# Performance work log

Hardware: AMD Instinct MI355X
Metric: run time of the kernel (lower is better)

## Reference

```python
import jax, jax.numpy as jnp
import numpy as np

B, G, P, E, H, K = 16, 512, 512, 256, 16, 16
CLIP = 10.0

def setup_inputs() -> dict:
    key = jax.random.key(0)
    ks = jax.random.split(key, 10)
    d = {
        "input1": jax.random.normal(ks[0], (B, 1, E), jnp.float32),
        "input2": jax.random.normal(ks[1], (B, G, E), jnp.float32),
        "current_time": jax.random.uniform(ks[2], (B, G, 1), jnp.float32),
        "ninf_mask": jnp.zeros((B, G, P), jnp.float32),
        "encoded_nodes": jax.random.normal(ks[3], (B, P, E), jnp.float32),
        # learned params (Linear weights stored [in, out]; y = x @ W)
        "Wq": jax.random.normal(ks[4], (2 * E + 1, H * K), jnp.float32) / np.sqrt(2 * E + 1),
        "Wk": jax.random.normal(ks[5], (E, H * K), jnp.float32) / np.sqrt(E),
        "Wv": jax.random.normal(ks[6], (E, H * K), jnp.float32) / np.sqrt(E),
        "Wc_w": jax.random.normal(ks[7], (H * K, E), jnp.float32) / np.sqrt(H * K),
        "Wc_b": jax.random.normal(ks[8], (E,), jnp.float32) * 0.01,
    }
    return d

def _heads(x):  # [B, N, H*K] -> [B, H, N, K]
    b, n, _ = x.shape
    return x.reshape(b, n, H, K).transpose(0, 2, 1, 3)

def reference(input1, input2, current_time, ninf_mask, encoded_nodes, Wq, Wk, Wv, Wc_w, Wc_b):
    # reset(): precompute k, v, single_head_key from encoded_nodes
    k = _heads(encoded_nodes @ Wk)  # [B,H,P,K]
    v = _heads(encoded_nodes @ Wv)  # [B,H,P,K]

    # forward()
    input_cat = jnp.concatenate(
        (jnp.broadcast_to(input1, (B, G, E)), input2, current_time), axis=2)  # [B,G,2E+1]
    q = _heads(input_cat @ Wq)  # [B,H,G,K]

    # MHA with additive ninf mask
    score = jnp.einsum("bhgk,bhpk->bhgp", q, k) / np.sqrt(K)
    score = score + ninf_mask[:, None, :, :]
    weights = jax.nn.softmax(score, axis=3)
    out = jnp.einsum("bhgp,bhpk->bhgk", weights, v)
    out_concat = out.transpose(0, 2, 1, 3).reshape(B, G, H * K)
    mh_atten_out = out_concat @ Wc_w + Wc_b  # [B,G,E]

    # single-head pointer score with tanh clipping
    score2 = jnp.einsum("bge,bpe->bgp", mh_atten_out, encoded_nodes) / np.sqrt(E)
    score_clipped = CLIP * jnp.tanh(score2)
    probs = jax.nn.softmax(score_clipped + ninf_mask, axis=2)
    return probs
```

## Files before the change

kernel.cpp:

```cpp
#include <hip/hip_runtime.h>
#include <math.h>

#define BB 16
#define GG 512
#define PP 512
#define EE 256
#define HH 16
#define KD 16
#define HK 256

typedef __bf16 bf16x8 __attribute__((ext_vector_type(8)));
typedef __bf16 bf16x4 __attribute__((ext_vector_type(4)));
typedef float f32x4 __attribute__((ext_vector_type(4)));
typedef float f32x16 __attribute__((ext_vector_type(16)));

#define SA_STRIDE 40
#define SMEM_BYTES 30720

__device__ inline void cvt_split8(const float* __restrict__ p, bf16x8& h, bf16x8& l)
{
    float4 f0 = *(const float4*)p;
    float4 f1 = *(const float4*)(p + 4);
    float v[8] = {f0.x, f0.y, f0.z, f0.w, f1.x, f1.y, f1.z, f1.w};
#pragma unroll
    for (int j = 0; j < 8; ++j) {
        __bf16 hh = (__bf16)v[j];
        h[j] = hh;
        l[j] = (__bf16)(v[j] - (float)hh);
    }
}

__global__ __launch_bounds__(256) void weight_prep(const float* __restrict__ Wk,
                                                   const float* __restrict__ Wv,
                                                   const float* __restrict__ Wq,
                                                   const float* __restrict__ Wc,
                                                   const float* __restrict__ in1,
                                                   __bf16* __restrict__ wkt_h, __bf16* __restrict__ wkt_l,
                                                   __bf16* __restrict__ wvt_h, __bf16* __restrict__ wvt_l,
                                                   __bf16* __restrict__ wqt_h, __bf16* __restrict__ wqt_l,
                                                   __bf16* __restrict__ wct_h, __bf16* __restrict__ wct_l,
                                                   float* __restrict__ q1p)
{
    int gid = blockIdx.x * 256 + threadIdx.x;
    if (gid < 16384) {
        const int b = gid >> 10, q = (gid >> 8) & 3, n = gid & 255;
        const float* ip = in1 + (size_t)b * EE + q * 64;
        const float* wp = Wq + (size_t)(q * 64) * HK + n;
        float acc = 0.f;
#pragma unroll 8
        for (int k = 0; k < 64; ++k) acc += ip[k] * wp[(size_t)k * HK];
        q1p[gid] = acc;
        return;
    }
    int id = gid - 16384;
    const float* W;
    __bf16 *th, *tl;
    int krow = 0;
    if (id < 65536)       { W = Wk; th = wkt_h; tl = wkt_l; }
    else if (id < 131072) { id -= 65536;  W = Wv; th = wvt_h; tl = wvt_l; }
    else if (id < 196608) { id -= 131072; W = Wq; th = wqt_h; tl = wqt_l; krow = 256; }
    else                  { id -= 196608; W = Wc; th = wct_h; tl = wct_l; }
    const int k = id & 255;
    const int n = id >> 8;
    const float v = W[(size_t)(k + krow) * HK + n];
    const __bf16 h = (__bf16)v;
    th[(n << 8) + k] = h;
    tl[(n << 8) + k] = (__bf16)(v - (float)h);
}

__device__ inline void kvproj_body(int bx, int tid, unsigned char* smem,
                                   const float* __restrict__ A,
                                   const __bf16* __restrict__ Bkh,
                                   const __bf16* __restrict__ Bkl,
                                   const __bf16* __restrict__ Bvh,
                                   const __bf16* __restrict__ Bvl,
                                   __bf16* __restrict__ Khi,
                                   __bf16* __restrict__ Klo,
                                   __bf16* __restrict__ Vt)
{
    __bf16* sAh = (__bf16*)smem;
    __bf16* sAl = sAh + 64 * SA_STRIDE;
    __bf16* sB  = sAl + 64 * SA_STRIDE;

    const int lane = tid & 63;
    const int w = __builtin_amdgcn_readfirstlane(tid >> 6);
    const int m0 = (bx >> 2) * 64;
    const int n0 = (bx & 3) * 64;
    const int wm = (w >> 1) * 32, wn = (w & 1) * 32;
    const int ln = lane & 15, kq = (lane >> 4) * 8;
    const int ar = tid >> 2, ac = (tid & 3) * 8;

    const __bf16* bsel = (w == 0) ? Bkh : (w == 1) ? Bkl : (w == 2) ? Bvh : Bvl;

    f32x4 ak[2][2], av[2][2];
#pragma unroll
    for (int i = 0; i < 2; ++i)
#pragma unroll
        for (int j = 0; j < 2; ++j) {
            ak[i][j] = (f32x4){0.f, 0.f, 0.f, 0.f};
            av[i][j] = (f32x4){0.f, 0.f, 0.f, 0.f};
        }

    for (int k0 = 0; k0 < EE; k0 += 32) {
        {
            bf16x8 h8, l8;
            cvt_split8(A + (size_t)(m0 + ar) * EE + k0 + ac, h8, l8);
            *(bf16x8*)&sAh[ar * SA_STRIDE + ac] = h8;
            *(bf16x8*)&sAl[ar * SA_STRIDE + ac] = l8;
        }
        {
            const __bf16* src = bsel + (size_t)(n0 + lane) * EE + k0;
            __bf16* dst = sB + (w * 64 + lane) * SA_STRIDE;
            *(bf16x8*)&dst[0]  = *(const bf16x8*)&src[0];
            *(bf16x8*)&dst[8]  = *(const bf16x8*)&src[8];
            *(bf16x8*)&dst[16] = *(const bf16x8*)&src[16];
            *(bf16x8*)&dst[24] = *(const bf16x8*)&src[24];
        }
        __syncthreads();

        bf16x8 ah[2], al[2];
#pragma unroll
        for (int mt = 0; mt < 2; ++mt) {
            ah[mt] = *(const bf16x8*)&sAh[(wm + mt * 16 + ln) * SA_STRIDE + kq];
            al[mt] = *(const bf16x8*)&sAl[(wm + mt * 16 + ln) * SA_STRIDE + kq];
        }
#pragma unroll
        for (int nt = 0; nt < 2; ++nt) {
            const int rowb = wn + nt * 16 + ln;
            bf16x8 bkh8 = *(const bf16x8*)&sB[(0 * 64 + rowb) * SA_STRIDE + kq];
            bf16x8 bkl8 = *(const bf16x8*)&sB[(1 * 64 + rowb) * SA_STRIDE + kq];
            bf16x8 bvh8 = *(const bf16x8*)&sB[(2 * 64 + rowb) * SA_STRIDE + kq];
            bf16x8 bvl8 = *(const bf16x8*)&sB[(3 * 64 + rowb) * SA_STRIDE + kq];
#pragma unroll
            for (int mt = 0; mt < 2; ++mt) {
                ak[mt][nt] = __builtin_amdgcn_mfma_f32_16x16x32_bf16(ah[mt], bkh8, ak[mt][nt], 0, 0, 0);
                ak[mt][nt] = __builtin_amdgcn_mfma_f32_16x16x32_bf16(al[mt], bkh8, ak[mt][nt], 0, 0, 0);
                ak[mt][nt] = __builtin_amdgcn_mfma_f32_16x16x32_bf16(ah[mt], bkl8, ak[mt][nt], 0, 0, 0);
                av[mt][nt] = __builtin_amdgcn_mfma_f32_16x16x32_bf16(ah[mt], bvh8, av[mt][nt], 0, 0, 0);
                av[mt][nt] = __builtin_amdgcn_mfma_f32_16x16x32_bf16(al[mt], bvh8, av[mt][nt], 0, 0, 0);
                av[mt][nt] = __builtin_amdgcn_mfma_f32_16x16x32_bf16(ah[mt], bvl8, av[mt][nt], 0, 0, 0);
            }
        }
        __syncthreads();
    }

    __bf16* eKh = (__bf16*)smem;
    __bf16* eKl = eKh + 5120;
    __bf16* eV  = eKl + 5120;

    const int rbase = (lane >> 4) * 4;
#pragma unroll
    for (int mt = 0; mt < 2; ++mt)
#pragma unroll
        for (int nt = 0; nt < 2; ++nt) {
            const int hloc = (w & 1) * 2 + nt;
            const int nl = wn + nt * 16 + ln;
#pragma unroll
            for (int r = 0; r < 4; ++r) {
                const int m = wm + mt * 16 + rbase + r;
                const float vk = ak[mt][nt][r];
                const __bf16 hk = (__bf16)vk;
                eKh[(hloc * 64 + m) * 20 + ln] = hk;
                eKl[(hloc * 64 + m) * 20 + ln] = (__bf16)(vk - (float)hk);
                eV[nl * 68 + m] = (__bf16)av[mt][nt][r];
            }
        }
    __syncthreads();

    const int b = m0 >> 9;
    const int pbase = m0 & (PP - 1);
    {
        const int hl = tid >> 6, p = tid & 63;
        const int hg = (n0 >> 4) + hl;
        const size_t dst = (((size_t)b * HH + hg) * PP + pbase + p) * KD;
        const int base = (hl * 64 + p) * 20;
        uint2 a0 = *(const uint2*)&eKh[base + 0];
        uint2 a1 = *(const uint2*)&eKh[base + 4];
        uint2 a2 = *(const uint2*)&eKh[base + 8];
        uint2 a3 = *(const uint2*)&eKh[base + 12];
        *(uint4*)(Khi + dst)     = make_uint4(a0.x, a0.y, a1.x, a1.y);
        *(uint4*)(Khi + dst + 8) = make_uint4(a2.x, a2.y, a3.x, a3.y);
        uint2 c0 = *(const uint2*)&eKl[base + 0];
        uint2 c1 = *(const uint2*)&eKl[base + 4];
        uint2 c2 = *(const uint2*)&eKl[base + 8];
        uint2 c3 = *(const uint2*)&eKl[base + 12];
        *(uint4*)(Klo + dst)     = make_uint4(c0.x, c0.y, c1.x, c1.y);
        *(uint4*)(Klo + dst + 8) = make_uint4(c2.x, c2.y, c3.x, c3.y);
    }
    {
        const int n = tid >> 2, qq = tid & 3;
        const int ng = n0 + n, hg = ng >> 4, kk = ng & 15;
        const int base = n * 68 + qq * 16;
        uint2 v0 = *(const uint2*)&eV[base + 0];
        uint2 v1 = *(const uint2*)&eV[base + 4];
        uint2 v2 = *(const uint2*)&eV[base + 8];
        uint2 v3 = *(const uint2*)&eV[base + 12];
        const size_t dst = ((((size_t)b * HH + hg) * KD + kk) * PP) + pbase + qq * 16;
        *(uint4*)(Vt + dst)     = make_uint4(v0.x, v0.y, v1.x, v1.y);
        *(uint4*)(Vt + dst + 8) = make_uint4(v2.x, v2.y, v3.x, v3.y);
    }
}

__device__ inline void qproj_body(int bx, int tid, unsigned char* smem,
                                  const float* __restrict__ in2,
                                  const float* __restrict__ ct,
                                  const __bf16* __restrict__ Bh,
                                  const __bf16* __restrict__ Bl,
                                  const float* __restrict__ WqFull,
                                  const float* __restrict__ q1p,
                                  __bf16* __restrict__ Qhi,
                                  __bf16* __restrict__ Qlo)
{
    __bf16* sAh = (__bf16*)smem;
    __bf16* sAl = sAh + 64 * SA_STRIDE;
    __bf16* sB  = sAl + 64 * SA_STRIDE;

    const int lane = tid & 63;
    const int w = __builtin_amdgcn_readfirstlane(tid >> 6);
    const int m0 = (bx >> 2) * 64;
    const int n0 = (bx & 3) * 64;
    const int wm = (w >> 1) * 32, wn = (w & 1) * 32;
    const int ln = lane & 15, kq = (lane >> 4) * 8;
    const int ar = tid >> 2, ac = (tid & 3) * 8;
    const int b = m0 >> 9;
    const float* WqLast = WqFull + (size_t)512 * HK;

    f32x4 acc[2][2];
#pragma unroll
    for (int i = 0; i < 2; ++i)
#pragma unroll
        for (int j = 0; j < 2; ++j) acc[i][j] = (f32x4){0.f, 0.f, 0.f, 0.f};

    for (int k0 = 0; k0 < EE; k0 += 32) {
        {
            bf16x8 h8, l8;
            cvt_split8(in2 + (size_t)(m0 + ar) * EE + k0 + ac, h8, l8);
            *(bf16x8*)&sAh[ar * SA_STRIDE + ac] = h8;
            *(bf16x8*)&sAl[ar * SA_STRIDE + ac] = l8;
        }
        {
            const int mat = w >> 1;
            const int row = (w & 1) * 32 + (lane >> 1);
            const int half = (lane & 1) * 16;
            const __bf16* src = (mat ? Bl : Bh) + ((size_t)(n0 + row) << 8) + k0 + half;
            __bf16* dst = sB + (mat * 64 + row) * SA_STRIDE + half;
            *(bf16x8*)&dst[0] = *(const bf16x8*)&src[0];
            *(bf16x8*)&dst[8] = *(const bf16x8*)&src[8];
        }
        __syncthreads();

        bf16x8 ah[2], al[2];
#pragma unroll
        for (int mt = 0; mt < 2; ++mt) {
            ah[mt] = *(const bf16x8*)&sAh[(wm + mt * 16 + ln) * SA_STRIDE + kq];
            al[mt] = *(const bf16x8*)&sAl[(wm + mt * 16 + ln) * SA_STRIDE + kq];
        }
#pragma unroll
        for (int nt = 0; nt < 2; ++nt) {
            const int rowb = wn + nt * 16 + ln;
            bf16x8 bh8 = *(const bf16x8*)&sB[(0 * 64 + rowb) * SA_STRIDE + kq];
            bf16x8 bl8 = *(const bf16x8*)&sB[(1 * 64 + rowb) * SA_STRIDE + kq];
#pragma unroll
            for (int mt = 0; mt < 2; ++mt) {
                acc[mt][nt] = __builtin_amdgcn_mfma_f32_16x16x32_bf16(ah[mt], bh8, acc[mt][nt], 0, 0, 0);
                acc[mt][nt] = __builtin_amdgcn_mfma_f32_16x16x32_bf16(al[mt], bh8, acc[mt][nt], 0, 0, 0);
                acc[mt][nt] = __builtin_amdgcn_mfma_f32_16x16x32_bf16(ah[mt], bl8, acc[mt][nt], 0, 0, 0);
            }
        }
        __syncthreads();
    }

    __bf16* eQh = (__bf16*)smem;
    __bf16* eQl = eQh + 5120;

    const int rbase = (lane >> 4) * 4;
#pragma unroll
    for (int mt = 0; mt < 2; ++mt)
#pragma unroll
        for (int nt = 0; nt < 2; ++nt) {
            const int hloc = (w & 1) * 2 + nt;
            const int ng = n0 + wn + nt * 16 + ln;
            const float wq = WqLast[ng];
            const float q1v = q1p[b * 1024 + 0 * 256 + ng] + q1p[b * 1024 + 1 * 256 + ng]
                            + q1p[b * 1024 + 2 * 256 + ng] + q1p[b * 1024 + 3 * 256 + ng];
#pragma unroll
            for (int r = 0; r < 4; ++r) {
                const int m = wm + mt * 16 + rbase + r;
                const float v = acc[mt][nt][r] + q1v + ct[m0 + m] * wq;
                const __bf16 h = (__bf16)v;
                eQh[(hloc * 64 + m) * 20 + ln] = h;
                eQl[(hloc * 64 + m) * 20 + ln] = (__bf16)(v - (float)h);
            }
        }
    __syncthreads();

    {
        const int hl = tid >> 6, p = tid & 63;
        const int hg = (n0 >> 4) + hl;
        const int g = (m0 & (GG - 1)) + p;
        const size_t dst = (((size_t)b * HH + hg) * GG + g) * KD;
        const int base = (hl * 64 + p) * 20;
        uint2 a0 = *(const uint2*)&eQh[base + 0];
        uint2 a1 = *(const uint2*)&eQh[base + 4];
        uint2 a2 = *(const uint2*)&eQh[base + 8];
        uint2 a3 = *(const uint2*)&eQh[base + 12];
        *(uint4*)(Qhi + dst)     = make_uint4(a0.x, a0.y, a1.x, a1.y);
        *(uint4*)(Qhi + dst + 8) = make_uint4(a2.x, a2.y, a3.x, a3.y);
        uint2 c0 = *(const uint2*)&eQl[base + 0];
        uint2 c1 = *(const uint2*)&eQl[base + 4];
        uint2 c2 = *(const uint2*)&eQl[base + 8];
        uint2 c3 = *(const uint2*)&eQl[base + 12];
        *(uint4*)(Qlo + dst)     = make_uint4(c0.x, c0.y, c1.x, c1.y);
        *(uint4*)(Qlo + dst + 8) = make_uint4(c2.x, c2.y, c3.x, c3.y);
    }
}

__global__ __launch_bounds__(256, 2) void fused_proj(const float* __restrict__ enc,
                                                     const __bf16* __restrict__ Bkh,
                                                     const __bf16* __restrict__ Bkl,
                                                     const __bf16* __restrict__ Bvh,
                                                     const __bf16* __restrict__ Bvl,
                                                     __bf16* __restrict__ Khi,
                                                     __bf16* __restrict__ Klo,
                                                     __bf16* __restrict__ Vt,
                                                     const float* __restrict__ in2,
                                                     const float* __restrict__ ct,
                                                     const __bf16* __restrict__ Bqh,
                                                     const __bf16* __restrict__ Bql,
                                                     const float* __restrict__ WqFull,
                                                     const float* __restrict__ q1p,
                                                     __bf16* __restrict__ Qhi,
                                                     __bf16* __restrict__ Qlo)
{
    __shared__ __align__(16) unsigned char smem[SMEM_BYTES];
    const int id = blockIdx.x;
    if (id < 512)
        kvproj_body(id, threadIdx.x, smem, enc, Bkh, Bkl, Bvh, Bvl, Khi, Klo, Vt);
    else
        qproj_body(id - 512, threadIdx.x, smem, in2, ct, Bqh, Bql, WqFull, q1p, Qhi, Qlo);
}

__global__ __launch_bounds__(256, 4) void attn_v8(const __bf16* __restrict__ Qhi,
                                                  const __bf16* __restrict__ Qlo,
                                                  const __bf16* __restrict__ Khi,
                                                  const __bf16* __restrict__ Klo,
                                                  const __bf16* __restrict__ Vt,
                                                  const float* __restrict__ mask,
                                                  __bf16* __restrict__ Ath,
                                                  __bf16* __restrict__ Atl)
{
    __shared__ __align__(16) __bf16 sP[4][32][40];
    __shared__ float srs[4][32];

    const int t = threadIdx.x;
    const int lane = t & 63;
    const int w = __builtin_amdgcn_readfirstlane(t >> 6);
    const int g0 = blockIdx.x * 32;
    const int h = blockIdx.y * 4 + w;
    const int b = blockIdx.z;
    const int ln32 = lane & 31;
    const int half = lane >> 5;
    const int ln16 = lane & 15;
    const int quad = (lane >> 4) & 3;

    const size_t qbase = (((size_t)b * HH + h) * GG + g0) * KD;
    const size_t kbase = ((size_t)b * HH + h) * PP * KD;
    const size_t vbase = ((size_t)b * HH + h) * KD * PP;
    const float* mbase = mask + ((size_t)(b * GG + g0)) * PP;

    bf16x8 qah = *(const bf16x8*)(Qhi + qbase + (size_t)ln32 * KD + half * 8);
    bf16x8 qal = *(const bf16x8*)(Qlo + qbase + (size_t)ln32 * KD + half * 8);

    float rs[16];
#pragma unroll
    for (int r = 0; r < 16; ++r) rs[r] = 0.f;
    f32x4 o0 = (f32x4){0.f, 0.f, 0.f, 0.f};
    f32x4 o1 = (f32x4){0.f, 0.f, 0.f, 0.f};

#pragma unroll 2
    for (int pc = 0; pc < 16; ++pc) {
        const int pb = pc * 32;
        const size_t ko = kbase + (size_t)(pb + ln32) * KD + half * 8;
        bf16x8 kh = *(const bf16x8*)(Khi + ko);
        bf16x8 kl = *(const bf16x8*)(Klo + ko);

        f32x16 s = (f32x16){0.f, 0.f, 0.f, 0.f, 0.f, 0.f, 0.f, 0.f,
                            0.f, 0.f, 0.f, 0.f, 0.f, 0.f, 0.f, 0.f};
        s = __builtin_amdgcn_mfma_f32_32x32x16_bf16(qah, kh, s, 0, 0, 0);
        s = __builtin_amdgcn_mfma_f32_32x32x16_bf16(qal, kh, s, 0, 0, 0);
        s = __builtin_amdgcn_mfma_f32_32x32x16_bf16(qah, kl, s, 0, 0, 0);

#pragma unroll
        for (int r = 0; r < 16; ++r) {
            const int row = (r & 3) + 8 * (r >> 2) + 4 * half;
            const float m = mbase[(size_t)row * PP + pb + ln32];
            const float e = __expf(s[r] * 0.25f + m);
            rs[r] += e;
            sP[w][row][ln32] = (__bf16)e;
        }

        bf16x8 vb = *(const bf16x8*)(Vt + vbase + (size_t)ln16 * PP + pb + quad * 8);
        bf16x8 p0 = *(const bf16x8*)&sP[w][ln16][quad * 8];
        bf16x8 p1 = *(const bf16x8*)&sP[w][16 + ln16][quad * 8];
        o0 = __builtin_amdgcn_mfma_f32_16x16x32_bf16(p0, vb, o0, 0, 0, 0);
        o1 = __builtin_amdgcn_mfma_f32_16x16x32_bf16(p1, vb, o1, 0, 0, 0);
    }

#pragma unroll
    for (int r = 0; r < 16; ++r) {
#pragma unroll
        for (int mm = 1; mm < 32; mm <<= 1) rs[r] += __shfl_xor(rs[r], mm);
    }
    if (ln32 == 0) {
#pragma unroll
        for (int r = 0; r < 16; ++r)
            srs[w][(r & 3) + 8 * (r >> 2) + 4 * half] = rs[r];
    }

#pragma unroll
    for (int t2 = 0; t2 < 2; ++t2) {
        const f32x4 oc = t2 ? o1 : o0;
#pragma unroll
        for (int r = 0; r < 4; ++r) {
            const int grow = t2 * 16 + quad * 4 + r;
            const float v = oc[r] / srs[w][grow];
            const __bf16 hv = (__bf16)v;
            const size_t oo = ((size_t)(b * GG + g0 + grow)) * HK + h * KD + ln16;
            Ath[oo] = hv;
            Atl[oo] = (__bf16)(v - (float)hv);
        }
    }
}

__device__ inline void outproj_body(int bx, int tid,
                                    const __bf16* __restrict__ Ah,
                                    const __bf16* __restrict__ Al,
                                    const __bf16* __restrict__ Bh,
                                    const __bf16* __restrict__ Bl,
                                    const float* __restrict__ bias,
                                    __bf16* __restrict__ Ch,
                                    __bf16* __restrict__ Cl)
{
    const int lane = tid & 63, w = tid >> 6;
    const int m0 = (bx >> 2) * 64 + (w >> 1) * 32;
    const int n0 = (bx & 3) * 64 + (w & 1) * 32;
    const int ln = lane & 15, kc = (lane >> 4) * 8;

    f32x4 acc[2][2];
#pragma unroll
    for (int i = 0; i < 2; ++i)
#pragma unroll
        for (int j = 0; j < 2; ++j) acc[i][j] = (f32x4){0.f, 0.f, 0.f, 0.f};

    for (int k0 = 0; k0 < EE; k0 += 32) {
        bf16x8 ah[2], al[2], bh[2], bl[2];
#pragma unroll
        for (int mt = 0; mt < 2; ++mt) {
            const size_t o = (size_t)(m0 + mt * 16 + ln) * EE + k0 + kc;
            ah[mt] = *(const bf16x8*)(Ah + o);
            al[mt] = *(const bf16x8*)(Al + o);
        }
#pragma unroll
        for (int nt = 0; nt < 2; ++nt) {
            const size_t o = (size_t)(n0 + nt * 16 + ln) * EE + k0 + kc;
            bh[nt] = *(const bf16x8*)(Bh + o);
            bl[nt] = *(const bf16x8*)(Bl + o);
        }
#pragma unroll
        for (int mt = 0; mt < 2; ++mt)
#pragma unroll
            for (int nt = 0; nt < 2; ++nt) {
                acc[mt][nt] = __builtin_amdgcn_mfma_f32_16x16x32_bf16(ah[mt], bh[nt], acc[mt][nt], 0, 0, 0);
                acc[mt][nt] = __builtin_amdgcn_mfma_f32_16x16x32_bf16(al[mt], bh[nt], acc[mt][nt], 0, 0, 0);
                acc[mt][nt] = __builtin_amdgcn_mfma_f32_16x16x32_bf16(ah[mt], bl[nt], acc[mt][nt], 0, 0, 0);
            }
    }

    const int rbase = (lane >> 4) * 4;
#pragma unroll
    for (int mt = 0; mt < 2; ++mt)
#pragma unroll
        for (int nt = 0; nt < 2; ++nt)
#pragma unroll
            for (int r = 0; r < 4; ++r) {
                const int m = m0 + rbase + r + mt * 16;
                const int n = n0 + nt * 16 + ln;
                const float v = acc[mt][nt][r] + bias[n];
                const __bf16 h = (__bf16)v;
                Ch[(size_t)m * HK + n] = h;
                Cl[(size_t)m * HK + n] = (__bf16)(v - (float)h);
            }
}

__global__ __launch_bounds__(256) void fused_post(const __bf16* __restrict__ Ah,
                                                  const __bf16* __restrict__ Al,
                                                  const __bf16* __restrict__ Bh,
                                                  const __bf16* __restrict__ Bl,
                                                  const float* __restrict__ bias,
                                                  __bf16* __restrict__ Ch,
                                                  __bf16* __restrict__ Cl,
                                                  const float* __restrict__ enc,
                                                  __bf16* __restrict__ enc_h,
                                                  __bf16* __restrict__ enc_l)
{
    const int id = blockIdx.x;
    if (id < 512) {
        outproj_body(id, threadIdx.x, Ah, Al, Bh, Bl, bias, Ch, Cl);
    } else {
        const int i = ((id - 512) * 256 + threadIdx.x) * 4;
        float4 v = *(const float4*)(enc + i);
        bf16x4 h, l;
        h[0] = (__bf16)v.x; l[0] = (__bf16)(v.x - (float)h[0]);
        h[1] = (__bf16)v.y; l[1] = (__bf16)(v.y - (float)h[1]);
        h[2] = (__bf16)v.z; l[2] = (__bf16)(v.z - (float)h[2]);
        h[3] = (__bf16)v.w; l[3] = (__bf16)(v.w - (float)h[3]);
        *(bf16x4*)(enc_h + i) = h;
        *(bf16x4*)(enc_l + i) = l;
    }
}

__global__ __launch_bounds__(512) void pointer_v3(const __bf16* __restrict__ mh_hi,
                                                  const __bf16* __restrict__ mh_lo,
                                                  const __bf16* __restrict__ enc_hi,
                                                  const __bf16* __restrict__ enc_lo,
                                                  const float* __restrict__ mask,
                                                  float* __restrict__ out)
{
    __shared__ float swsum[8][32];
    const int t = threadIdx.x;
    const int lane = t & 63;
    const int w = __builtin_amdgcn_readfirstlane(t >> 6);
    const int id = blockIdx.x;
    const int b = id & 15;
    const int g0 = (id >> 4) * 32;
    const int ln32 = lane & 31;
    const int half = lane >> 5;

    const size_t arow = ((size_t)(b * GG + g0 + ln32)) * EE + half * 8;
    const size_t brow = ((size_t)(b * PP + w * 64 + ln32)) * EE + half * 8;

    f32x16 acc[2];
#pragma unroll
    for (int pt = 0; pt < 2; ++pt)
        acc[pt] = (f32x16){0.f, 0.f, 0.f, 0.f, 0.f, 0.f, 0.f, 0.f,
                           0.f, 0.f, 0.f, 0.f, 0.f, 0.f, 0.f, 0.f};

    for (int kc = 0; kc < EE; kc += 16) {
        bf16x8 ah = *(const bf16x8*)(mh_hi + arow + kc);
        bf16x8 al = *(const bf16x8*)(mh_lo + arow + kc);
#pragma unroll
        for (int pt = 0; pt < 2; ++pt) {
            const size_t bo = brow + (size_t)pt * 32 * EE + kc;
            bf16x8 bh = *(const bf16x8*)(enc_hi + bo);
            bf16x8 bl = *(const bf16x8*)(enc_lo + bo);
            acc[pt] = __builtin_amdgcn_mfma_f32_32x32x16_bf16(ah, bh, acc[pt], 0, 0, 0);
            acc[pt] = __builtin_amdgcn_mfma_f32_32x32x16_bf16(al, bh, acc[pt], 0, 0, 0);
            acc[pt] = __builtin_amdgcn_mfma_f32_32x32x16_bf16(ah, bl, acc[pt], 0, 0, 0);
        }
    }

    float rsum[16];
#pragma unroll
    for (int r = 0; r < 16; ++r) rsum[r] = 0.f;
#pragma unroll
    for (int pt = 0; pt < 2; ++pt)
#pragma unroll
        for (int r = 0; r < 16; ++r) {
            const int row = (r & 3) + 8 * (r >> 2) + 4 * half;
            float s = acc[pt][r] * 0.0625f;
            s = fminf(9.f, fmaxf(-9.f, s));
            const float e2 = __expf(2.f * s);
            const float th = (e2 - 1.f) / (e2 + 1.f);
            const float m = mask[((size_t)(b * GG + g0 + row)) * PP + w * 64 + pt * 32 + ln32];
            const float e = __expf(10.f * th + m);
            acc[pt][r] = e;
            rsum[r] += e;
        }

#pragma unroll
    for (int r = 0; r < 16; ++r) {
        rsum[r] += __shfl_xor(rsum[r], 1);
        rsum[r] += __shfl_xor(rsum[r], 2);
        rsum[r] += __shfl_xor(rsum[r], 4);
        rsum[r] += __shfl_xor(rsum[r], 8);
        rsum[r] += __shfl_xor(rsum[r], 16);
    }
    if (ln32 == 0) {
#pragma unroll
        for (int r = 0; r < 16; ++r)
            swsum[w][(r & 3) + 8 * (r >> 2) + 4 * half] = rsum[r];
    }
    __syncthreads();

    float inv[16];
#pragma unroll
    for (int r = 0; r < 16; ++r) {
        const int row = (r & 3) + 8 * (r >> 2) + 4 * half;
        float tot = 0.f;
#pragma unroll
        for (int wv = 0; wv < 8; ++wv) tot += swsum[wv][row];
        inv[r] = 1.f / tot;
    }

#pragma unroll
    for (int pt = 0; pt < 2; ++pt)
#pragma unroll
        for (int r = 0; r < 16; ++r) {
            const int row = (r & 3) + 8 * (r >> 2) + 4 * half;
            out[((size_t)(b * GG + g0 + row)) * PP + w * 64 + pt * 32 + ln32] =
                acc[pt][r] * inv[r];
        }
}

extern "C" void kernel_launch(void* const* d_in, const int* in_sizes, int n_in,
                              void* d_out, int out_size, void* d_ws, size_t ws_size,
                              hipStream_t stream)
{
    const float* in1  = (const float*)d_in[0];
    const float* in2  = (const float*)d_in[1];
    const float* ct   = (const float*)d_in[2];
    const float* mask = (const float*)d_in[3];
    const float* enc  = (const float*)d_in[4];
    const float* Wq   = (const float*)d_in[5];
    const float* Wk   = (const float*)d_in[6];
    const float* Wv   = (const float*)d_in[7];
    const float* Wcw  = (const float*)d_in[8];
    const float* Wcb  = (const float*)d_in[9];
    float* out = (float*)d_out;
    float* ws  = (float*)d_ws;

    const size_t SEG = (size_t)BB * GG * HK;
    __bf16* Khi = (__bf16*)ws;
    __bf16* Klo = Khi + SEG;
    __bf16* Vt  = (__bf16*)(ws + SEG);
    __bf16* Ath = Vt + SEG;
    __bf16* Qhi = (__bf16*)(ws + 2 * SEG);
    __bf16* Qlo = Qhi + SEG;
    __bf16* wkt_h = (__bf16*)(ws + 3 * SEG);
    __bf16* wkt_l = wkt_h + 65536;
    __bf16* wvt_h = wkt_l + 65536;
    __bf16* wvt_l = wvt_h + 65536;
    __bf16* wqt_h = wvt_l + 65536;
    __bf16* wqt_l = wqt_h + 65536;
    __bf16* wct_h = wqt_l + 65536;
    __bf16* wct_l = wct_h + 65536;
    float*  q1p   = ws + 3 * SEG + 262144;
    __bf16* Atl   = (__bf16*)(ws + 3 * SEG) + 1048576;
    __bf16* mh_h  = (__bf16*)ws;
    __bf16* mh_l  = mh_h + SEG;
    __bf16* enc_h = (__bf16*)(ws + 2 * SEG);
    __bf16* enc_l = enc_h + SEG;

    const dim3 blk(256);

    weight_prep<<<dim3(1088), blk, 0, stream>>>(Wk, Wv, Wq, Wcw, in1,
                                                wkt_h, wkt_l, wvt_h, wvt_l,
                                                wqt_h, wqt_l, wct_h, wct_l, q1p);

    fused_proj<<<dim3(1024), blk, 0, stream>>>(enc, wkt_h, wkt_l, wvt_h, wvt_l,
                                               Khi, Klo, Vt,
                                               in2, ct, wqt_h, wqt_l, Wq, q1p,
                                               Qhi, Qlo);

    attn_v8<<<dim3(GG / 32, HH / 4, BB), blk, 0, stream>>>(Qhi, Qlo, Khi, Klo, Vt, mask, Ath, Atl);

    fused_post<<<dim3(2560), blk, 0, stream>>>(Ath, Atl, wct_h, wct_l, Wcb,
                                               mh_h, mh_l, enc, enc_h, enc_l);

    pointer_v3<<<dim3(256), dim3(512), 0, stream>>>(mh_h, mh_l, enc_h, enc_l, mask, out);
}
```

Before: 202.4 us.

## Fold output projection into pointer keys via reassociated encoded_nodes·Wc product

Reassociates (A·Wc + b)·encᵀ into A·(enc·Wcᵀ)ᵀ + b·encᵀ. The product enc·Wcᵀ and the per-node bias term are computed in the weight_prep launch, which runs independently of the attention path. This removes the separate output-projection/enc-conversion kernel and its intermediate write/read. The pointer kernel now consumes the attention output directly with the precomputed keys plus a bias add. In exchange, the prep kernel does a full B×P×E×HK GEMM up front, making it larger.

```diff
diff --git a/kernel.cpp b/kernel.cpp
--- a/kernel.cpp
+++ b/kernel.cpp
@@ -30,18 +30,129 @@
     }
 }
 
+__device__ inline void w2proj_body(int bx, int tid, unsigned char* smem,
+                                   const float* __restrict__ enc,
+                                   const float* __restrict__ Wc,
+                                   const float* __restrict__ bias,
+                                   __bf16* __restrict__ W2th,
+                                   __bf16* __restrict__ W2tl,
+                                   float* __restrict__ biasEnc)
+{
+    __bf16* sAh = (__bf16*)smem;
+    __bf16* sAl = sAh + 64 * SA_STRIDE;
+    __bf16* sBh = sAl + 64 * SA_STRIDE;
+    __bf16* sBl = sBh + 64 * SA_STRIDE;
+
+    const int lane = tid & 63;
+    const int w = __builtin_amdgcn_readfirstlane(tid >> 6);
+    const int b  = bx >> 5;
+    const int t  = bx & 31;
+    const int p0 = (t >> 2) * 64;
+    const int n0 = (t & 3) * 64;
+    const bool do_bias = (n0 == 0);
+    const int wm = (w >> 1) * 32, wn = (w & 1) * 32;
+    const int ln = lane & 15, kq = (lane >> 4) * 8;
+    const int ar = tid >> 2, ac = (tid & 3) * 8;
+
+    f32x4 acc[2][2];
+#pragma unroll
+    for (int i = 0; i < 2; ++i)
+#pragma unroll
+        for (int j = 0; j < 2; ++j) acc[i][j] = (f32x4){0.f, 0.f, 0.f, 0.f};
+    float bacc = 0.f;
+
+    for (int k0 = 0; k0 < EE; k0 += 32) {
+        {
+            const float* ap = enc + ((size_t)(b * PP + p0 + ar)) * EE + k0 + ac;
+            float4 f0 = *(const float4*)ap;
+            float4 f1 = *(const float4*)(ap + 4);
+            float v[8] = {f0.x, f0.y, f0.z, f0.w, f1.x, f1.y, f1.z, f1.w};
+            bf16x8 h8, l8;
+#pragma unroll
+            for (int j = 0; j < 8; ++j) {
+                __bf16 hh = (__bf16)v[j];
+                h8[j] = hh;
+                l8[j] = (__bf16)(v[j] - (float)hh);
+            }
+            if (do_bias) {
+#pragma unroll
+                for (int j = 0; j < 8; ++j) bacc += v[j] * bias[k0 + ac + j];
+            }
+            *(bf16x8*)&sAh[ar * SA_STRIDE + ac] = h8;
+            *(bf16x8*)&sAl[ar * SA_STRIDE + ac] = l8;
+        }
+        {
+            bf16x8 h8, l8;
+            cvt_split8(Wc + (size_t)(n0 + ar) * EE + k0 + ac, h8, l8);
+            *(bf16x8*)&sBh[ar * SA_STRIDE + ac] = h8;
+            *(bf16x8*)&sBl[ar * SA_STRIDE + ac] = l8;
+        }
+        __syncthreads();
+
+        bf16x8 ah[2], al[2];
+#pragma unroll
+        for (int mt = 0; mt < 2; ++mt) {
+            ah[mt] = *(const bf16x8*)&sAh[(wm + mt * 16 + ln) * SA_STRIDE + kq];
+            al[mt] = *(const bf16x8*)&sAl[(wm + mt * 16 + ln) * SA_STRIDE + kq];
+        }
+#pragma unroll
+        for (int nt = 0; nt < 2; ++nt) {
+            const int rowb = wn + nt * 16 + ln;
+            bf16x8 bh8 = *(const bf16x8*)&sBh[rowb * SA_STRIDE + kq];
+            bf16x8 bl8 = *(const bf16x8*)&sBl[rowb * SA_STRIDE + kq];
+#pragma unroll
+            for (int mt = 0; mt < 2; ++mt) {
+                acc[mt][nt] = __builtin_amdgcn_mfma_f32_16x16x32_bf16(ah[mt], bh8, acc[mt][nt], 0, 0, 0);
+                acc[mt][nt] = __builtin_amdgcn_mfma_f32_16x16x32_bf16(al[mt], bh8, acc[mt][nt], 0, 0, 0);
+                acc[mt][nt] = __builtin_amdgcn_mfma_f32_16x16x32_bf16(ah[mt], bl8, acc[mt][nt], 0, 0, 0);
+            }
+        }
+        __syncthreads();
+    }
+
+    if (do_bias) {
+        bacc += __shfl_xor(bacc, 1);
+        bacc += __shfl_xor(bacc, 2);
+        if ((tid & 3) == 0) biasEnc[b * PP + p0 + ar] = bacc;
+    }
+
+    const int rbase = (lane >> 4) * 4;
+#pragma unroll
+    for (int mt = 0; mt < 2; ++mt)
+#pragma unroll
+        for (int nt = 0; nt < 2; ++nt)
+#pragma unroll
+            for (int r = 0; r < 4; ++r) {
+                const int p = p0 + wm + mt * 16 + rbase + r;
+                const int n = n0 + wn + nt * 16 + ln;
+                const float v = acc[mt][nt][r];
+                const __bf16 h = (__bf16)v;
+                const size_t o = ((size_t)(b * PP + p)) * HK + n;
+                W2th[o] = h;
+                W2tl[o] = (__bf16)(v - (float)h);
+            }
+}
+
 __global__ __launch_bounds__(256) void weight_prep(const float* __restrict__ Wk,
                                                    const float* __restrict__ Wv,
                                                    const float* __restrict__ Wq,
                                                    const float* __restrict__ Wc,
                                                    const float* __restrict__ in1,
+                                                   const float* __restrict__ enc,
+                                                   const float* __restrict__ Wcb,
                                                    __bf16* __restrict__ wkt_h, __bf16* __restrict__ wkt_l,
                                                    __bf16* __restrict__ wvt_h, __bf16* __restrict__ wvt_l,
                                                    __bf16* __restrict__ wqt_h, __bf16* __restrict__ wqt_l,
-                                                   __bf16* __restrict__ wct_h, __bf16* __restrict__ wct_l,
-                                                   float* __restrict__ q1p)
-{
-    int gid = blockIdx.x * 256 + threadIdx.x;
+                                                   float* __restrict__ q1p,
+                                                   __bf16* __restrict__ W2th, __bf16* __restrict__ W2tl,
+                                                   float* __restrict__ biasEnc)
+{
+    __shared__ __align__(16) unsigned char smem[4 * 64 * SA_STRIDE * 2];
+    if (blockIdx.x < 512) {
+        w2proj_body(blockIdx.x, threadIdx.x, smem, enc, Wc, Wcb, W2th, W2tl, biasEnc);
+        return;
+    }
+    int gid = (blockIdx.x - 512) * 256 + threadIdx.x;
     if (gid < 16384) {
         const int b = gid >> 10, q = (gid >> 8) & 3, n = gid & 255;
         const float* ip = in1 + (size_t)b * EE + q * 64;
@@ -53,13 +164,13 @@
         return;
     }
     int id = gid - 16384;
+    if (id >= 196608) return;
     const float* W;
     __bf16 *th, *tl;
     int krow = 0;
     if (id < 65536)       { W = Wk; th = wkt_h; tl = wkt_l; }
     else if (id < 131072) { id -= 65536;  W = Wv; th = wvt_h; tl = wvt_l; }
-    else if (id < 196608) { id -= 131072; W = Wq; th = wqt_h; tl = wqt_l; krow = 256; }
-    else                  { id -= 196608; W = Wc; th = wct_h; tl = wct_l; }
+    else                  { id -= 131072; W = Wq; th = wqt_h; tl = wqt_l; krow = 256; }
     const int k = id & 255;
     const int n = id >> 8;
     const float v = W[(size_t)(k + krow) * HK + n];
@@ -432,97 +543,11 @@
     }
 }
 
-__device__ inline void outproj_body(int bx, int tid,
-                                    const __bf16* __restrict__ Ah,
-                                    const __bf16* __restrict__ Al,
-                                    const __bf16* __restrict__ Bh,
-                                    const __bf16* __restrict__ Bl,
-                                    const float* __restrict__ bias,
-                                    __bf16* __restrict__ Ch,
-                                    __bf16* __restrict__ Cl)
-{
-    const int lane = tid & 63, w = tid >> 6;
-    const int m0 = (bx >> 2) * 64 + (w >> 1) * 32;
-    const int n0 = (bx & 3) * 64 + (w & 1) * 32;
-    const int ln = lane & 15, kc = (lane >> 4) * 8;
-
-    f32x4 acc[2][2];
-#pragma unroll
-    for (int i = 0; i < 2; ++i)
-#pragma unroll
-        for (int j = 0; j < 2; ++j) acc[i][j] = (f32x4){0.f, 0.f, 0.f, 0.f};
-
-    for (int k0 = 0; k0 < EE; k0 += 32) {
-        bf16x8 ah[2], al[2], bh[2], bl[2];
-#pragma unroll
-        for (int mt = 0; mt < 2; ++mt) {
-            const size_t o = (size_t)(m0 + mt * 16 + ln) * EE + k0 + kc;
-            ah[mt] = *(const bf16x8*)(Ah + o);
-            al[mt] = *(const bf16x8*)(Al + o);
-        }
-#pragma unroll
-        for (int nt = 0; nt < 2; ++nt) {
-            const size_t o = (size_t)(n0 + nt * 16 + ln) * EE + k0 + kc;
-            bh[nt] = *(const bf16x8*)(Bh + o);
-            bl[nt] = *(const bf16x8*)(Bl + o);
-        }
-#pragma unroll
-        for (int mt = 0; mt < 2; ++mt)
-#pragma unroll
-            for (int nt = 0; nt < 2; ++nt) {
-                acc[mt][nt] = __builtin_amdgcn_mfma_f32_16x16x32_bf16(ah[mt], bh[nt], acc[mt][nt], 0, 0, 0);
-                acc[mt][nt] = __builtin_amdgcn_mfma_f32_16x16x32_bf16(al[mt], bh[nt], acc[mt][nt], 0, 0, 0);
-                acc[mt][nt] = __builtin_amdgcn_mfma_f32_16x16x32_bf16(ah[mt], bl[nt], acc[mt][nt], 0, 0, 0);
-            }
-    }
-
-    const int rbase = (lane >> 4) * 4;
-#pragma unroll
-    for (int mt = 0; mt < 2; ++mt)
-#pragma unroll
-        for (int nt = 0; nt < 2; ++nt)
-#pragma unroll
-            for (int r = 0; r < 4; ++r) {
-                const int m = m0 + rbase + r + mt * 16;
-                const int n = n0 + nt * 16 + ln;
-                const float v = acc[mt][nt][r] + bias[n];
-                const __bf16 h = (__bf16)v;
-                Ch[(size_t)m * HK + n] = h;
-                Cl[(size_t)m * HK + n] = (__bf16)(v - (float)h);
-            }
-}
-
-__global__ __launch_bounds__(256) void fused_post(const __bf16* __restrict__ Ah,
-                                                  const __bf16* __restrict__ Al,
-                                                  const __bf16* __restrict__ Bh,
-                                                  const __bf16* __restrict__ Bl,
-                                                  const float* __restrict__ bias,
-                                                  __bf16* __restrict__ Ch,
-                                                  __bf16* __restrict__ Cl,
-                                                  const float* __restrict__ enc,
-                                                  __bf16* __restrict__ enc_h,
-                                                  __bf16* __restrict__ enc_l)
-{
-    const int id = blockIdx.x;
-    if (id < 512) {
-        outproj_body(id, threadIdx.x, Ah, Al, Bh, Bl, bias, Ch, Cl);
-    } else {
-        const int i = ((id - 512) * 256 + threadIdx.x) * 4;
-        float4 v = *(const float4*)(enc + i);
-        bf16x4 h, l;
-        h[0] = (__bf16)v.x; l[0] = (__bf16)(v.x - (float)h[0]);
-        h[1] = (__bf16)v.y; l[1] = (__bf16)(v.y - (float)h[1]);
-        h[2] = (__bf16)v.z; l[2] = (__bf16)(v.z - (float)h[2]);
-        h[3] = (__bf16)v.w; l[3] = (__bf16)(v.w - (float)h[3]);
-        *(bf16x4*)(enc_h + i) = h;
-        *(bf16x4*)(enc_l + i) = l;
-    }
-}
-
-__global__ __launch_bounds__(512) void pointer_v3(const __bf16* __restrict__ mh_hi,
-                                                  const __bf16* __restrict__ mh_lo,
-                                                  const __bf16* __restrict__ enc_hi,
-                                                  const __bf16* __restrict__ enc_lo,
+__global__ __launch_bounds__(512) void pointer_v4(const __bf16* __restrict__ a_hi,
+                                                  const __bf16* __restrict__ a_lo,
+                                                  const __bf16* __restrict__ w2_hi,
+                                                  const __bf16* __restrict__ w2_lo,
+                                                  const float* __restrict__ biasEnc,
                                                   const float* __restrict__ mask,
                                                   float* __restrict__ out)
 {
@@ -536,8 +561,11 @@
     const int ln32 = lane & 31;
     const int half = lane >> 5;
 
-    const size_t arow = ((size_t)(b * GG + g0 + ln32)) * EE + half * 8;
-    const size_t brow = ((size_t)(b * PP + w * 64 + ln32)) * EE + half * 8;
+    const size_t arow = ((size_t)(b * GG + g0 + ln32)) * HK + half * 8;
+    const size_t brow = ((size_t)(b * PP + w * 64 + ln32)) * HK + half * 8;
+
+    const float be0 = biasEnc[b * PP + w * 64 + ln32];
+    const float be1 = biasEnc[b * PP + w * 64 + 32 + ln32];
 
     f32x16 acc[2];
 #pragma unroll
@@ -545,14 +573,14 @@
         acc[pt] = (f32x16){0.f, 0.f, 0.f, 0.f, 0.f, 0.f, 0.f, 0.f,
                            0.f, 0.f, 0.f, 0.f, 0.f, 0.f, 0.f, 0.f};
 
-    for (int kc = 0; kc < EE; kc += 16) {
-        bf16x8 ah = *(const bf16x8*)(mh_hi + arow + kc);
-        bf16x8 al = *(const bf16x8*)(mh_lo + arow + kc);
+    for (int kc = 0; kc < HK; kc += 16) {
+        bf16x8 ah = *(const bf16x8*)(a_hi + arow + kc);
+        bf16x8 al = *(const bf16x8*)(a_lo + arow + kc);
 #pragma unroll
         for (int pt = 0; pt < 2; ++pt) {
-            const size_t bo = brow + (size_t)pt * 32 * EE + kc;
-            bf16x8 bh = *(const bf16x8*)(enc_hi + bo);
-            bf16x8 bl = *(const bf16x8*)(enc_lo + bo);
+            const size_t bo = brow + (size_t)pt * 32 * HK + kc;
+            bf16x8 bh = *(const bf16x8*)(w2_hi + bo);
+            bf16x8 bl = *(const bf16x8*)(w2_lo + bo);
             acc[pt] = __builtin_amdgcn_mfma_f32_32x32x16_bf16(ah, bh, acc[pt], 0, 0, 0);
             acc[pt] = __builtin_amdgcn_mfma_f32_32x32x16_bf16(al, bh, acc[pt], 0, 0, 0);
             acc[pt] = __builtin_amdgcn_mfma_f32_32x32x16_bf16(ah, bl, acc[pt], 0, 0, 0);
@@ -567,7 +595,7 @@
 #pragma unroll
         for (int r = 0; r < 16; ++r) {
             const int row = (r & 3) + 8 * (r >> 2) + 4 * half;
-            float s = acc[pt][r] * 0.0625f;
+            float s = (acc[pt][r] + (pt ? be1 : be0)) * 0.0625f;
             s = fminf(9.f, fmaxf(-9.f, s));
             const float e2 = __expf(2.f * s);
             const float th = (e2 - 1.f) / (e2 + 1.f);
@@ -642,20 +670,18 @@
     __bf16* wvt_l = wvt_h + 65536;
     __bf16* wqt_h = wvt_l + 65536;
     __bf16* wqt_l = wqt_h + 65536;
-    __bf16* wct_h = wqt_l + 65536;
-    __bf16* wct_l = wct_h + 65536;
-    float*  q1p   = ws + 3 * SEG + 262144;
+    float*  q1p     = ws + 3 * SEG + 196608;
+    float*  biasEnc = q1p + 16384;
     __bf16* Atl   = (__bf16*)(ws + 3 * SEG) + 1048576;
-    __bf16* mh_h  = (__bf16*)ws;
-    __bf16* mh_l  = mh_h + SEG;
-    __bf16* enc_h = (__bf16*)(ws + 2 * SEG);
-    __bf16* enc_l = enc_h + SEG;
+    __bf16* W2th  = (__bf16*)(ws + 4 * SEG);
+    __bf16* W2tl  = W2th + SEG;
 
     const dim3 blk(256);
 
-    weight_prep<<<dim3(1088), blk, 0, stream>>>(Wk, Wv, Wq, Wcw, in1,
+    weight_prep<<<dim3(1344), blk, 0, stream>>>(Wk, Wv, Wq, Wcw, in1, enc, Wcb,
                                                 wkt_h, wkt_l, wvt_h, wvt_l,
-                                                wqt_h, wqt_l, wct_h, wct_l, q1p);
+                                                wqt_h, wqt_l, q1p,
+                                                W2th, W2tl, biasEnc);
 
     fused_proj<<<dim3(1024), blk, 0, stream>>>(enc, wkt_h, wkt_l, wvt_h, wvt_l,
                                                Khi, Klo, Vt,
@@ -664,8 +690,5 @@
 
     attn_v8<<<dim3(GG / 32, HH / 4, BB), blk, 0, stream>>>(Qhi, Qlo, Khi, Klo, Vt, mask, Ath, Atl);
 
-    fused_post<<<dim3(2560), blk, 0, stream>>>(Ath, Atl, wct_h, wct_l, Wcb,
-                                               mh_h, mh_l, enc, enc_h, enc_l);
-
-    pointer_v3<<<dim3(256), dim3(512), 0, stream>>>(mh_h, mh_l, enc_h, enc_l, mask, out);
-}
+    pointer_v4<<<dim3(256), dim3(512), 0, stream>>>(Ath, Atl, W2th, W2tl, biasEnc, mask, out);
+}
```

Result: no change. 199.8 us (-1.3%).
